# Optimization experiments

Hardware: AMD Instinct MI355X
Metric: run time of the kernel (lower is better)

The kernel has to match this reference:

```python
import jax, jax.numpy as jnp
import numpy as np

B, N, X, H = 128, 512, 128, 256  # batch, seq len, in features, hidden

_PARAM_SHAPES = [
    ("fg_w_c", (H,)), ("fg_w_h", (H, H)), ("fg_w_x", (H, X)), ("fg_b", (H,)),
    ("ig_w_c", (H,)), ("ig_w_h", (H, H)), ("ig_w_x", (H, X)), ("ig_b", (H,)),
    ("in_w_h", (H, H)), ("in_w_x", (H, X)), ("in_b", (H,)),
    ("og_w_cn", (H,)), ("og_w_h", (H, H)), ("og_w_x", (H, X)), ("og_b", (H,)), ("og_w_t", (H,)),
    ("tg1_w_x", (H, X)), ("tg1_w_t", (H,)), ("tg1_b", (H,)),
    ("tg2_w_x", (H, X)), ("tg2_w_t", (H,)), ("tg2_b", (H,)),
]


def setup_inputs() -> dict:
    key = jax.random.key(0)
    ks = jax.random.split(key, 2 + len(_PARAM_SHAPES))
    stdv = 1.0 / np.sqrt(H)  # torch __init__ re-inits all params uniform(-stdv, stdv)
    inp = {
        "x": jax.random.normal(ks[0], (B, N, X), jnp.float32),
        "t": jax.random.uniform(ks[1], (B, N, 1), jnp.float32),  # time intervals >= 0
    }
    for i, (name, shape) in enumerate(_PARAM_SHAPES):
        inp[name] = jax.random.uniform(ks[2 + i], shape, jnp.float32, -stdv, stdv)
    return inp


def reference(x, t,
              fg_w_c, fg_w_h, fg_w_x, fg_b,
              ig_w_c, ig_w_h, ig_w_x, ig_b,
              in_w_h, in_w_x, in_b,
              og_w_cn, og_w_h, og_w_x, og_b, og_w_t,
              tg1_w_x, tg1_w_t, tg1_b,
              tg2_w_x, tg2_w_t, tg2_b):
    # TimeLSTM_v3 with nn_type = NN_TYPE_LSTM_TIME2.
    # torch stores vector params as [H,1] and x_cur as [B,xm,1]; here squeezed to [H] / [B,xm].
    # Precompute all input-dependent (non-recurrent) gate terms over the whole sequence: [B,N,H]
    fg_x = jnp.einsum('bnx,hx->bnh', x, fg_w_x) + fg_b
    ig_x = jnp.einsum('bnx,hx->bnh', x, ig_w_x) + ig_b
    in_x = jnp.einsum('bnx,hx->bnh', x, in_w_x) + in_b
    og_x = jnp.einsum('bnx,hx->bnh', x, og_w_x) + og_w_t * t + og_b
    # Time gates depend only on x and t -> fully precomputable
    tm1 = jax.nn.sigmoid(jnp.einsum('bnx,hx->bnh', x, tg1_w_x) + jnp.tanh(tg1_w_t * t) + tg1_b)
    tm2 = jax.nn.sigmoid(jnp.einsum('bnx,hx->bnh', x, tg2_w_x) + jnp.tanh(tg2_w_t * t) + tg2_b)

    def step(carry, inputs):
        h, cm = carry  # each [B,H]
        fg_xt, ig_xt, in_xt, og_xt, tm1_t, tm2_t = inputs
        ig = jax.nn.sigmoid(ig_w_c * cm + h @ ig_w_h.T + ig_xt)
        fg = jax.nn.sigmoid(fg_w_c * cm + h @ fg_w_h.T + fg_xt)
        inn = jnp.tanh(h @ in_w_h.T + in_xt)
        cm_hat = fg * cm + ig * tm1_t * inn
        cm_new = fg * cm + ig * tm2_t * inn
        og = jax.nn.sigmoid(og_w_cn * cm_hat + h @ og_w_h.T + og_xt)
        h_new = og * jnp.tanh(cm_hat)
        return (h_new, cm_new), None

    seqs = tuple(jnp.moveaxis(a, 1, 0) for a in (fg_x, ig_x, in_x, og_x, tm1, tm2))  # [N,B,H]
    init = (jnp.zeros((x.shape[0], H), x.dtype), jnp.zeros((x.shape[0], H), x.dtype))
    (h, cm), _ = jax.lax.scan(step, init, seqs)
    return h, cm  # h: [B,H] (torch squeezes trailing 1), cm: [B,H]
```

## Files before the change

### kernel.cpp

```cpp
#include <hip/hip_runtime.h>
#include <math.h>

#define BATCH 128
#define SEQN  512
#define XF    128
#define HF    256
#define BC    16
#define HC    8
#define TCH   8
#define NBLK  256
#define NTHR  256
#define NGRP  8
#define GSZ   32

#define OFF_WX   0
#define OFF_G    6144
#define OFF_X    12288
#define OFF_CM   28672
#define OFF_TV   28800
#define OFF_COEF 28928
#define OFF_GO   29024
#define LDS_WORDS 29028
#define LDS_BYTES (LDS_WORDS * 4)

struct Params {
  const float* x;
  const float* t;
  const float* w_h[4];
  const float* w_x[6];
  const float* coef[12];
  float* h_buf;
  unsigned* flags;
  float* out;
};

__device__ __forceinline__ float sigmoidf_(float v) { return 1.0f / (1.0f + __expf(-v)); }

__device__ __forceinline__ float swzx1(float v) { return __int_as_float(__builtin_amdgcn_ds_swizzle(__float_as_int(v), 0x041F)); }
__device__ __forceinline__ float swzx2(float v) { return __int_as_float(__builtin_amdgcn_ds_swizzle(__float_as_int(v), 0x081F)); }
__device__ __forceinline__ float swzx4(float v) { return __int_as_float(__builtin_amdgcn_ds_swizzle(__float_as_int(v), 0x101F)); }
__device__ __forceinline__ float swzx8(float v) { return __int_as_float(__builtin_amdgcn_ds_swizzle(__float_as_int(v), 0x201F)); }

__device__ __forceinline__ void post_arrive(unsigned* flags, int gi, int mi, unsigned val) {
  __syncthreads();
  if (threadIdx.x == 0) {
    __hip_atomic_store(&flags[(gi * GSZ + mi) * 16], val,
                       __ATOMIC_RELAXED, __HIP_MEMORY_SCOPE_AGENT);
  }
}

__device__ __forceinline__ void wave_wait(float* sm, const unsigned* flags,
                                          int gi, unsigned target) {
  unsigned* go = (unsigned*)&sm[OFF_GO];
  const int tid = threadIdx.x;
  if (tid < 64) {
    const bool need = tid < GSZ;
    const unsigned* f = &flags[(gi * GSZ + (tid & (GSZ - 1))) * 16];
    while (true) {
      unsigned v = need ? __hip_atomic_load(f, __ATOMIC_RELAXED, __HIP_MEMORY_SCOPE_AGENT)
                        : target;
      if (__all((int)(v >= target))) break;
    }
    if (tid == 0)
      __hip_atomic_store(go, target, __ATOMIC_RELAXED, __HIP_MEMORY_SCOPE_WORKGROUP);
  } else {
    while (__hip_atomic_load(go, __ATOMIC_RELAXED, __HIP_MEMORY_SCOPE_WORKGROUP) < target) {}
  }
  asm volatile("" ::: "memory");
}

__global__ __launch_bounds__(NTHR, 1) void timelstm_kernel(Params p) {
  extern __shared__ float sm[];
  const int tid = threadIdx.x;
  const int bid = blockIdx.x;
  const int gi = bid & 7;
  const int mi = bid >> 3;
  const int b0 = gi * BC;
  const int h0 = mi * HC;

  const int lane = tid & 63;
  const int bq = tid >> 6;
  const int kh = lane & 7;
  const int j  = lane >> 3;

  float wrs[4][32];
#pragma unroll
  for (int g = 0; g < 4; ++g)
#pragma unroll
    for (int q = 0; q < 8; ++q) {
      const float4 v = *(const float4*)&p.w_h[g][(size_t)(h0 + j) * HF + kh * 32 + q * 4];
      wrs[g][q * 4 + 0] = v.x; wrs[g][q * 4 + 1] = v.y;
      wrs[g][q * 4 + 2] = v.z; wrs[g][q * 4 + 3] = v.w;
    }
  for (int i = tid; i < 6 * 8 * 128; i += NTHR) {
    int g = i >> 10, jj = (i >> 7) & 7, k = i & 127;
    sm[OFF_WX + k * 48 + jj * 6 + g] = p.w_x[g][(h0 + jj) * XF + k];
  }
  if (tid < 96) sm[OFF_COEF + tid] = p.coef[tid >> 3][h0 + (tid & 7)];
  if (tid < 128) sm[OFF_CM + tid] = 0.0f;
  if (tid == 0) *(unsigned*)&sm[OFF_GO] = 0u;
  if (mi == 0) {
    unsigned long long* hbu = (unsigned long long*)p.h_buf + (size_t)b0 * (HF / 2);
    for (int i = tid; i < BC * HF / 2; i += NTHR) {
      __hip_atomic_store(&hbu[i], 0ull, __ATOMIC_RELAXED, __HIP_MEMORY_SCOPE_AGENT);
    }
  }
  post_arrive(p.flags, gi, mi, 1u);
  unsigned tstep = 1;
  int cur = 0;

  for (int tc0 = 0; tc0 < SEQN; tc0 += TCH) {
    __syncthreads();
    {
#pragma unroll
      for (int half = 0; half < 2; ++half) {
        float4 xr[8];
#pragma unroll
        for (int it = 0; it < 8; ++it) {
          const int ri = (half * 8 + it) * 8 + (tid >> 5);
          xr[it] = *(const float4*)&p.x[((size_t)(b0 + (ri >> 3)) * SEQN + (tc0 + (ri & 7))) * XF + (tid & 31) * 4];
        }
#pragma unroll
        for (int it = 0; it < 8; ++it) {
          const int ri = (half * 8 + it) * 8 + (tid >> 5);
          const int k0 = (tid & 31) * 4;
          const float xb[4] = {xr[it].x, xr[it].y, xr[it].z, xr[it].w};
#pragma unroll
          for (int u = 0; u < 4; ++u) {
            const int k = k0 + u;
            sm[OFF_X + k * 128 + (ri ^ (((k >> 2) & 7) << 2))] = xb[u];
          }
        }
      }
      if (tid < 128)
        sm[OFF_TV + tid] = p.t[(size_t)(b0 + (tid >> 3)) * SEQN + tc0 + (tid & 7)];
    }
    __syncthreads();
    {
      const int c = tid >> 3, r = tid & 7;
      const int c4 = c << 2;
      float a0[4], a1[4], a2[4], a3[4], a4[4], a5[4];
#pragma unroll
      for (int u = 0; u < 4; ++u) { a0[u]=0.f; a1[u]=0.f; a2[u]=0.f; a3[u]=0.f; a4[u]=0.f; a5[u]=0.f; }
      const float* wxp = &sm[OFF_WX + r * 6];
#pragma unroll 4
      for (int k = 0; k < XF; ++k) {
        const float4 xv = *(const float4*)&sm[OFF_X + k * 128 + (c4 ^ (((k >> 2) & 7) << 2))];
        const float2 wA = *(const float2*)&wxp[k * 48 + 0];
        const float2 wB = *(const float2*)&wxp[k * 48 + 2];
        const float2 wC = *(const float2*)&wxp[k * 48 + 4];
        const float xs[4] = {xv.x, xv.y, xv.z, xv.w};
#pragma unroll
        for (int u = 0; u < 4; ++u) {
          a0[u] += wA.x * xs[u]; a1[u] += wA.y * xs[u];
          a2[u] += wB.x * xs[u]; a3[u] += wB.y * xs[u];
          a4[u] += wC.x * xs[u]; a5[u] += wC.y * xs[u];
        }
      }
      const float cfg  = sm[OFF_COEF + 0 * 8 + r], cig  = sm[OFF_COEF + 1 * 8 + r];
      const float cin  = sm[OFF_COEF + 2 * 8 + r];
      const float cogb = sm[OFF_COEF + 3 * 8 + r], cogwt = sm[OFF_COEF + 4 * 8 + r];
      const float ct1w = sm[OFF_COEF + 5 * 8 + r], ct1b = sm[OFF_COEF + 6 * 8 + r];
      const float ct2w = sm[OFF_COEF + 7 * 8 + r], ct2b = sm[OFF_COEF + 8 * 8 + r];
#pragma unroll
      for (int u = 0; u < 4; ++u) {
        const int bt = c4 + u, b = bt >> 3, t = bt & 7;
        const float tv = sm[OFF_TV + bt];
        float* gp = &sm[OFF_G + t * 768 + b * 8 + r];
        gp[0]   = a0[u] + cfg;
        gp[128] = a1[u] + cig;
        gp[256] = a2[u] + cin;
        gp[384] = a3[u] + cogwt * tv + cogb;
        gp[512] = sigmoidf_(a4[u] + tanhf(ct1w * tv) + ct1b);
        gp[640] = sigmoidf_(a5[u] + tanhf(ct2w * tv) + ct2b);
      }
    }
    __syncthreads();

    for (int tt = 0; tt < TCH; ++tt) {
      wave_wait(sm, p.flags, gi, tstep);
      {
        const unsigned long long* hsrc = (const unsigned long long*)
            (p.h_buf + (size_t)cur * BATCH * HF + (size_t)(b0 + (bq << 2)) * HF);
        unsigned long long v[4][2];
#pragma unroll
        for (int u = 0; u < 4; ++u) {
          const unsigned long long* src = hsrc + (size_t)u * (HF / 2) + lane * 2;
          v[u][0] = __hip_atomic_load(src,     __ATOMIC_RELAXED, __HIP_MEMORY_SCOPE_AGENT);
          v[u][1] = __hip_atomic_load(src + 1, __ATOMIC_RELAXED, __HIP_MEMORY_SCOPE_AGENT);
        }
        float f[4][4];
#pragma unroll
        for (int u = 0; u < 4; ++u) {
          union { unsigned long long u64; float2 f2; } c0, c1;
          c0.u64 = v[u][0]; c1.u64 = v[u][1];
          f[u][0] = c0.f2.x; f[u][1] = c0.f2.y; f[u][2] = c1.f2.x; f[u][3] = c1.f2.y;
        }
        const int swz = ((lane >> 3) & 7) << 2;
        const int wbase = OFF_X + (bq << 10);
#pragma unroll
        for (int e = 0; e < 4; ++e) {
          const int a = wbase + (((lane << 4) + (e << 2)) ^ swz);
          float2 lo = {f[0][e], f[1][e]};
          float2 hi = {f[2][e], f[3][e]};
          *(float2*)&sm[a]     = lo;
          *(float2*)&sm[a + 2] = hi;
        }
      }

      float acc[4][4];
#pragma unroll
      for (int bi = 0; bi < 4; ++bi)
#pragma unroll
        for (int g = 0; g < 4; ++g) acc[bi][g] = 0.f;

      const int hbase = OFF_X + (bq << 10) + (kh << 7);
      const int khx = kh << 2;
#pragma unroll
      for (int kk = 0; kk < 32; ++kk) {
        const int off = ((((kk & 7) << 2) ^ khx)) + ((kk >> 3) << 5);
        const float4 hv = *(const float4*)&sm[hbase + off];
        const float w0 = wrs[0][kk], w1 = wrs[1][kk], w2 = wrs[2][kk], w3 = wrs[3][kk];
        acc[0][0] += hv.x * w0; acc[0][1] += hv.x * w1; acc[0][2] += hv.x * w2; acc[0][3] += hv.x * w3;
        acc[1][0] += hv.y * w0; acc[1][1] += hv.y * w1; acc[1][2] += hv.y * w2; acc[1][3] += hv.y * w3;
        acc[2][0] += hv.z * w0; acc[2][1] += hv.z * w1; acc[2][2] += hv.z * w2; acc[2][3] += hv.z * w3;
        acc[3][0] += hv.w * w0; acc[3][1] += hv.w * w1; acc[3][2] += hv.w * w2; acc[3][3] += hv.w * w3;
      }

      const int kb0 = kh & 1, kb1 = (kh >> 1) & 1;
      float s1[2][4];
#pragma unroll
      for (int pp = 0; pp < 2; ++pp)
#pragma unroll
        for (int g = 0; g < 4; ++g) {
          const float mine  = kb0 ? acc[2 * pp + 1][g] : acc[2 * pp][g];
          const float yours = kb0 ? acc[2 * pp][g]     : acc[2 * pp + 1][g];
          s1[pp][g] = mine + swzx1(yours);
        }
      float s2[4];
#pragma unroll
      for (int g = 0; g < 4; ++g) {
        const float mine  = kb1 ? s1[1][g] : s1[0][g];
        const float yours = kb1 ? s1[0][g] : s1[1][g];
        s2[g] = mine + swzx2(yours);
      }
      float pre[4];
#pragma unroll
      for (int g = 0; g < 4; ++g) pre[g] = s2[g] + swzx4(s2[g]);

      {
        const int bi = kh & 3;
        const int b  = (bq << 2) + bi;
        const int ib = b * 8 + j;
        const float cm = sm[OFF_CM + ib];
        const float* gt = &sm[OFF_G + tt * 768 + ib];
        const float fgx = gt[0],   igx = gt[128], inx = gt[256];
        const float ogx = gt[384], tm1 = gt[512], tm2 = gt[640];
        const float igv = sigmoidf_(sm[OFF_COEF + 10 * 8 + j] * cm + pre[1] + igx);
        const float fgv = sigmoidf_(sm[OFF_COEF + 9 * 8 + j] * cm + pre[0] + fgx);
        const float inn = tanhf(pre[2] + inx);
        const float cbase = fgv * cm, cinn = igv * inn;
        const float cmh = cbase + cinn * tm1;
        const float cmn = cbase + cinn * tm2;
        const float ogv = sigmoidf_(sm[OFF_COEF + 11 * 8 + j] * cmh + pre[3] + ogx);
        const float hn  = ogv * tanhf(cmh);
        const float hn2 = swzx8(hn);
        if (kh < 4) {
          sm[OFF_CM + ib] = cmn;
          if (!(j & 1)) {
            union { float2 f; unsigned long long u; } cv;
            cv.f.x = hn; cv.f.y = hn2;
            unsigned long long* hdst =
                (unsigned long long*)(p.h_buf + (size_t)(cur ^ 1) * BATCH * HF +
                                      (size_t)(b0 + b) * HF + h0 + j);
            __hip_atomic_store(hdst, cv.u, __ATOMIC_RELAXED, __HIP_MEMORY_SCOPE_AGENT);
          }
          if (tc0 + tt == SEQN - 1) {
            p.out[(size_t)(b0 + b) * HF + h0 + j] = hn;
            p.out[(size_t)BATCH * HF + (size_t)(b0 + b) * HF + h0 + j] = cmn;
          }
        }
      }
      post_arrive(p.flags, gi, mi, tstep + 1);
      ++tstep;
      cur ^= 1;
    }
  }
}

extern "C" void kernel_launch(void* const* d_in, const int* in_sizes, int n_in,
                              void* d_out, int out_size, void* d_ws, size_t ws_size,
                              hipStream_t stream) {
  (void)in_sizes; (void)n_in; (void)out_size; (void)ws_size;
  Params p;
  p.x = (const float*)d_in[0];
  p.t = (const float*)d_in[1];
  p.w_h[0] = (const float*)d_in[3];
  p.w_h[1] = (const float*)d_in[7];
  p.w_h[2] = (const float*)d_in[10];
  p.w_h[3] = (const float*)d_in[14];
  p.w_x[0] = (const float*)d_in[4];
  p.w_x[1] = (const float*)d_in[8];
  p.w_x[2] = (const float*)d_in[11];
  p.w_x[3] = (const float*)d_in[15];
  p.w_x[4] = (const float*)d_in[18];
  p.w_x[5] = (const float*)d_in[21];
  p.coef[0]  = (const float*)d_in[5];
  p.coef[1]  = (const float*)d_in[9];
  p.coef[2]  = (const float*)d_in[12];
  p.coef[3]  = (const float*)d_in[16];
  p.coef[4]  = (const float*)d_in[17];
  p.coef[5]  = (const float*)d_in[19];
  p.coef[6]  = (const float*)d_in[20];
  p.coef[7]  = (const float*)d_in[22];
  p.coef[8]  = (const float*)d_in[23];
  p.coef[9]  = (const float*)d_in[2];
  p.coef[10] = (const float*)d_in[6];
  p.coef[11] = (const float*)d_in[13];
  p.flags = (unsigned*)d_ws;
  p.h_buf = (float*)((char*)d_ws + 32768);
  p.out = (float*)d_out;

  (void)hipMemsetAsync(d_ws, 0, 16384, stream);
  (void)hipFuncSetAttribute((const void*)timelstm_kernel,
                            hipFuncAttributeMaxDynamicSharedMemorySize, LDS_BYTES);
  timelstm_kernel<<<dim3(NBLK), dim3(NTHR), LDS_BYTES, stream>>>(p);
}
```

Baseline: 2.613 ms.

## Overlap next-chunk input projection with inter-block spin waits

Before, the kernel stopped the recurrence at the start of every 8-step chunk to load x and compute the input-gate projections. Now that work is split into 20 slices: x/t loads first, then 8-wide k-chunks of the projection GEMV. Each wave runs pending slices while it spins on the cross-block step flags, so it does useful work during synchronisation idle time instead of at a separate barrier-fenced phase. x staging gets its own LDS region, separate from the h buffer, so both can be live at once. tanhf is also replaced by an exp-based fast tanh. The slices read LDS data written by other waves with no workgroup barrier between them, which risks ordering races, and the fast tanh slightly changes accuracy.

```diff
diff --git a/kernel.cpp b/kernel.cpp
--- a/kernel.cpp
+++ b/kernel.cpp
@@ -12,15 +12,16 @@
 #define NTHR  256
 #define NGRP  8
 #define GSZ   32
+#define NS    20
 
 #define OFF_WX   0
 #define OFF_G    6144
-#define OFF_X    12288
-#define OFF_CM   28672
-#define OFF_TV   28800
-#define OFF_COEF 28928
-#define OFF_GO   29024
-#define LDS_WORDS 29028
+#define OFF_XS   12288
+#define OFF_H    28672
+#define OFF_CM   32768
+#define OFF_COEF 32896
+#define OFF_GO   32992
+#define LDS_WORDS 32996
 #define LDS_BYTES (LDS_WORDS * 4)
 
 struct Params {
@@ -35,6 +36,10 @@
 };
 
 __device__ __forceinline__ float sigmoidf_(float v) { return 1.0f / (1.0f + __expf(-v)); }
+__device__ __forceinline__ float tanhf_(float x) {
+  const float e = __expf(2.0f * x);
+  return 1.0f - 2.0f / (e + 1.0f);
+}
 
 __device__ __forceinline__ float swzx1(float v) { return __int_as_float(__builtin_amdgcn_ds_swizzle(__float_as_int(v), 0x041F)); }
 __device__ __forceinline__ float swzx2(float v) { return __int_as_float(__builtin_amdgcn_ds_swizzle(__float_as_int(v), 0x081F)); }
@@ -47,26 +52,6 @@
     __hip_atomic_store(&flags[(gi * GSZ + mi) * 16], val,
                        __ATOMIC_RELAXED, __HIP_MEMORY_SCOPE_AGENT);
   }
-}
-
-__device__ __forceinline__ void wave_wait(float* sm, const unsigned* flags,
-                                          int gi, unsigned target) {
-  unsigned* go = (unsigned*)&sm[OFF_GO];
-  const int tid = threadIdx.x;
-  if (tid < 64) {
-    const bool need = tid < GSZ;
-    const unsigned* f = &flags[(gi * GSZ + (tid & (GSZ - 1))) * 16];
-    while (true) {
-      unsigned v = need ? __hip_atomic_load(f, __ATOMIC_RELAXED, __HIP_MEMORY_SCOPE_AGENT)
-                        : target;
-      if (__all((int)(v >= target))) break;
-    }
-    if (tid == 0)
-      __hip_atomic_store(go, target, __ATOMIC_RELAXED, __HIP_MEMORY_SCOPE_WORKGROUP);
-  } else {
-    while (__hip_atomic_load(go, __ATOMIC_RELAXED, __HIP_MEMORY_SCOPE_WORKGROUP) < target) {}
-  }
-  asm volatile("" ::: "memory");
 }
 
 __global__ __launch_bounds__(NTHR, 1) void timelstm_kernel(Params p) {
@@ -106,46 +91,51 @@
     }
   }
   post_arrive(p.flags, gi, mi, 1u);
-  unsigned tstep = 1;
-  int cur = 0;
-
-  for (int tc0 = 0; tc0 < SEQN; tc0 += TCH) {
-    __syncthreads();
-    {
-#pragma unroll
-      for (int half = 0; half < 2; ++half) {
-        float4 xr[8];
-#pragma unroll
-        for (int it = 0; it < 8; ++it) {
-          const int ri = (half * 8 + it) * 8 + (tid >> 5);
-          xr[it] = *(const float4*)&p.x[((size_t)(b0 + (ri >> 3)) * SEQN + (tc0 + (ri & 7))) * XF + (tid & 31) * 4];
-        }
-#pragma unroll
-        for (int it = 0; it < 8; ++it) {
-          const int ri = (half * 8 + it) * 8 + (tid >> 5);
-          const int k0 = (tid & 31) * 4;
-          const float xb[4] = {xr[it].x, xr[it].y, xr[it].z, xr[it].w};
-#pragma unroll
-          for (int u = 0; u < 4; ++u) {
-            const int k = k0 + u;
-            sm[OFF_X + k * 128 + (ri ^ (((k >> 2) & 7) << 2))] = xb[u];
-          }
-        }
-      }
-      if (tid < 128)
-        sm[OFF_TV + tid] = p.t[(size_t)(b0 + (tid >> 3)) * SEQN + tc0 + (tid & 7)];
-    }
-    __syncthreads();
-    {
-      const int c = tid >> 3, r = tid & 7;
-      const int c4 = c << 2;
-      float a0[4], a1[4], a2[4], a3[4], a4[4], a5[4];
-#pragma unroll
-      for (int u = 0; u < 4; ++u) { a0[u]=0.f; a1[u]=0.f; a2[u]=0.f; a3[u]=0.f; a4[u]=0.f; a5[u]=0.f; }
-      const float* wxp = &sm[OFF_WX + r * 6];
-#pragma unroll 4
-      for (int k = 0; k < XF; ++k) {
-        const float4 xv = *(const float4*)&sm[OFF_X + k * 128 + (c4 ^ (((k >> 2) & 7) << 2))];
+
+  float a0[4], a1[4], a2[4], a3[4], a4[4], a5[4];
+  float tvr[4];
+#pragma unroll
+  for (int u = 0; u < 4; ++u) { a0[u]=0.f; a1[u]=0.f; a2[u]=0.f; a3[u]=0.f; a4[u]=0.f; a5[u]=0.f; }
+  int tc_next = 0;
+  int sc = 0;
+  const int cc = tid >> 3, rr = tid & 7;
+  const int c4 = cc << 2;
+
+  auto do_slice = [&](int s) {
+    if (s < 4) {
+      if (s == 0) {
+#pragma unroll
+        for (int u = 0; u < 4; ++u) {
+          const int bt = c4 + u;
+          tvr[u] = p.t[(size_t)(b0 + (bt >> 3)) * SEQN + tc_next + (bt & 7)];
+        }
+      }
+      float4 xr[4];
+#pragma unroll
+      for (int q = 0; q < 4; ++q) {
+        const int it = s * 4 + q;
+        const int bt = (bq << 5) + it * 2 + (lane >> 5);
+        xr[q] = *(const float4*)&p.x[((size_t)(b0 + (bt >> 3)) * SEQN + (tc_next + (bt & 7))) * XF + (lane & 31) * 4];
+      }
+#pragma unroll
+      for (int q = 0; q < 4; ++q) {
+        const int it = s * 4 + q;
+        const int bt = (bq << 5) + it * 2 + (lane >> 5);
+        const int k0 = (lane & 31) * 4;
+        const float xb[4] = {xr[q].x, xr[q].y, xr[q].z, xr[q].w};
+#pragma unroll
+        for (int u = 0; u < 4; ++u) {
+          const int k = k0 + u;
+          sm[OFF_XS + k * 128 + (bt ^ (((k >> 2) & 7) << 2))] = xb[u];
+        }
+      }
+    } else {
+      const float* wxp = &sm[OFF_WX + rr * 6];
+      const int kbase = (s - 4) * 8;
+#pragma unroll
+      for (int kk = 0; kk < 8; ++kk) {
+        const int k = kbase + kk;
+        const float4 xv = *(const float4*)&sm[OFF_XS + k * 128 + (c4 ^ (((k >> 2) & 7) << 2))];
         const float2 wA = *(const float2*)&wxp[k * 48 + 0];
         const float2 wB = *(const float2*)&wxp[k * 48 + 2];
         const float2 wC = *(const float2*)&wxp[k * 48 + 4];
@@ -157,28 +147,65 @@
           a4[u] += wC.x * xs[u]; a5[u] += wC.y * xs[u];
         }
       }
-      const float cfg  = sm[OFF_COEF + 0 * 8 + r], cig  = sm[OFF_COEF + 1 * 8 + r];
-      const float cin  = sm[OFF_COEF + 2 * 8 + r];
-      const float cogb = sm[OFF_COEF + 3 * 8 + r], cogwt = sm[OFF_COEF + 4 * 8 + r];
-      const float ct1w = sm[OFF_COEF + 5 * 8 + r], ct1b = sm[OFF_COEF + 6 * 8 + r];
-      const float ct2w = sm[OFF_COEF + 7 * 8 + r], ct2b = sm[OFF_COEF + 8 * 8 + r];
-#pragma unroll
-      for (int u = 0; u < 4; ++u) {
-        const int bt = c4 + u, b = bt >> 3, t = bt & 7;
-        const float tv = sm[OFF_TV + bt];
-        float* gp = &sm[OFF_G + t * 768 + b * 8 + r];
-        gp[0]   = a0[u] + cfg;
-        gp[128] = a1[u] + cig;
-        gp[256] = a2[u] + cin;
-        gp[384] = a3[u] + cogwt * tv + cogb;
-        gp[512] = sigmoidf_(a4[u] + tanhf(ct1w * tv) + ct1b);
-        gp[640] = sigmoidf_(a5[u] + tanhf(ct2w * tv) + ct2b);
-      }
-    }
-    __syncthreads();
+    }
+  };
+
+  auto dump_G = [&]() {
+    const float cfg  = sm[OFF_COEF + 0 * 8 + rr], cig  = sm[OFF_COEF + 1 * 8 + rr];
+    const float cin  = sm[OFF_COEF + 2 * 8 + rr];
+    const float cogb = sm[OFF_COEF + 3 * 8 + rr], cogwt = sm[OFF_COEF + 4 * 8 + rr];
+    const float ct1w = sm[OFF_COEF + 5 * 8 + rr], ct1b = sm[OFF_COEF + 6 * 8 + rr];
+    const float ct2w = sm[OFF_COEF + 7 * 8 + rr], ct2b = sm[OFF_COEF + 8 * 8 + rr];
+#pragma unroll
+    for (int u = 0; u < 4; ++u) {
+      const int bt = c4 + u, b = bt >> 3, t = bt & 7;
+      const float tv = tvr[u];
+      float* gp = &sm[OFF_G + t * 768 + b * 8 + rr];
+      gp[0]   = a0[u] + cfg;
+      gp[128] = a1[u] + cig;
+      gp[256] = a2[u] + cin;
+      gp[384] = a3[u] + cogwt * tv + cogb;
+      gp[512] = sigmoidf_(a4[u] + tanhf_(ct1w * tv) + ct1b);
+      gp[640] = sigmoidf_(a5[u] + tanhf_(ct2w * tv) + ct2b);
+      a0[u] = 0.f; a1[u] = 0.f; a2[u] = 0.f; a3[u] = 0.f; a4[u] = 0.f; a5[u] = 0.f;
+    }
+  };
+
+  auto wave_wait_s = [&](unsigned target) {
+    unsigned* go = (unsigned*)&sm[OFF_GO];
+    if (tid < 64) {
+      const bool need = tid < GSZ;
+      const unsigned* f = &p.flags[(gi * GSZ + (tid & (GSZ - 1))) * 16];
+      while (true) {
+        unsigned v = need ? __hip_atomic_load(f, __ATOMIC_RELAXED, __HIP_MEMORY_SCOPE_AGENT)
+                          : target;
+        if (__all((int)(v >= target))) break;
+        if (sc < NS) { do_slice(sc); ++sc; }
+      }
+      if (tid == 0)
+        __hip_atomic_store(go, target, __ATOMIC_RELAXED, __HIP_MEMORY_SCOPE_WORKGROUP);
+    } else {
+      while (true) {
+        unsigned v = __hip_atomic_load(go, __ATOMIC_RELAXED, __HIP_MEMORY_SCOPE_WORKGROUP);
+        if (v >= target) break;
+        if (sc < NS) { do_slice(sc); ++sc; }
+      }
+    }
+    asm volatile("" ::: "memory");
+  };
+
+  for (int s = 0; s < NS; ++s) do_slice(s);
+  dump_G();
+
+  unsigned tstep = 1;
+  int cur = 0;
+
+  for (int tc0 = 0; tc0 < SEQN; tc0 += TCH) {
+    tc_next = tc0 + TCH;
+    sc = (tc_next < SEQN) ? 0 : NS;
 
     for (int tt = 0; tt < TCH; ++tt) {
-      wave_wait(sm, p.flags, gi, tstep);
+      wave_wait_s(tstep);
       {
         const unsigned long long* hsrc = (const unsigned long long*)
             (p.h_buf + (size_t)cur * BATCH * HF + (size_t)(b0 + (bq << 2)) * HF);
@@ -192,12 +219,12 @@
         float f[4][4];
 #pragma unroll
         for (int u = 0; u < 4; ++u) {
-          union { unsigned long long u64; float2 f2; } c0, c1;
-          c0.u64 = v[u][0]; c1.u64 = v[u][1];
-          f[u][0] = c0.f2.x; f[u][1] = c0.f2.y; f[u][2] = c1.f2.x; f[u][3] = c1.f2.y;
+          union { unsigned long long u64; float2 f2; } x0, x1;
+          x0.u64 = v[u][0]; x1.u64 = v[u][1];
+          f[u][0] = x0.f2.x; f[u][1] = x0.f2.y; f[u][2] = x1.f2.x; f[u][3] = x1.f2.y;
         }
         const int swz = ((lane >> 3) & 7) << 2;
-        const int wbase = OFF_X + (bq << 10);
+        const int wbase = OFF_H + (bq << 10);
 #pragma unroll
         for (int e = 0; e < 4; ++e) {
           const int a = wbase + (((lane << 4) + (e << 2)) ^ swz);
@@ -214,7 +241,7 @@
 #pragma unroll
         for (int g = 0; g < 4; ++g) acc[bi][g] = 0.f;
 
-      const int hbase = OFF_X + (bq << 10) + (kh << 7);
+      const int hbase = OFF_H + (bq << 10) + (kh << 7);
       const int khx = kh << 2;
 #pragma unroll
       for (int kk = 0; kk < 32; ++kk) {
@@ -258,12 +285,12 @@
         const float ogx = gt[384], tm1 = gt[512], tm2 = gt[640];
         const float igv = sigmoidf_(sm[OFF_COEF + 10 * 8 + j] * cm + pre[1] + igx);
         const float fgv = sigmoidf_(sm[OFF_COEF + 9 * 8 + j] * cm + pre[0] + fgx);
-        const float inn = tanhf(pre[2] + inx);
+        const float inn = tanhf_(pre[2] + inx);
         const float cbase = fgv * cm, cinn = igv * inn;
         const float cmh = cbase + cinn * tm1;
         const float cmn = cbase + cinn * tm2;
         const float ogv = sigmoidf_(sm[OFF_COEF + 11 * 8 + j] * cmh + pre[3] + ogx);
-        const float hn  = ogv * tanhf(cmh);
+        const float hn  = ogv * tanhf_(cmh);
         const float hn2 = swzx8(hn);
         if (kh < 4) {
           sm[OFF_CM + ib] = cmn;
@@ -284,6 +311,11 @@
       post_arrive(p.flags, gi, mi, tstep + 1);
       ++tstep;
       cur ^= 1;
+    }
+
+    if (tc_next < SEQN) {
+      while (sc < NS) { do_slice(sc); ++sc; }
+      dump_G();
     }
   }
 }
```

Measured after the change: 2.874 ms. 10.0% more time.

## Use leader-block round counter for group barrier and fast exp-based tanh

Applied to the files above, without the earlier changes.

Per-step group synchronization changes from every block polling all 32 peer flags to only the mi==0 block polling them. That block then publishes a per-group round counter, and the other blocks spin on that single word. This cuts the polling traffic on the flags but adds an extra hop of latency through the leader block on the critical recurrence path. It also replaces tanhf with an __expf-based tanh to shorten the gate math, at some cost in accuracy and overflow behaviour for large inputs.

```diff
diff --git a/kernel.cpp b/kernel.cpp
--- a/kernel.cpp
+++ b/kernel.cpp
@@ -31,10 +31,15 @@
   const float* coef[12];
   float* h_buf;
   unsigned* flags;
+  unsigned* round;
   float* out;
 };
 
 __device__ __forceinline__ float sigmoidf_(float v) { return 1.0f / (1.0f + __expf(-v)); }
+__device__ __forceinline__ float tanhf_(float x) {
+  const float e = __expf(2.0f * x);
+  return 1.0f - 2.0f / (e + 1.0f);
+}
 
 __device__ __forceinline__ float swzx1(float v) { return __int_as_float(__builtin_amdgcn_ds_swizzle(__float_as_int(v), 0x041F)); }
 __device__ __forceinline__ float swzx2(float v) { return __int_as_float(__builtin_amdgcn_ds_swizzle(__float_as_int(v), 0x081F)); }
@@ -50,21 +55,30 @@
 }
 
 __device__ __forceinline__ void wave_wait(float* sm, const unsigned* flags,
-                                          int gi, unsigned target) {
-  unsigned* go = (unsigned*)&sm[OFF_GO];
+                                          unsigned* round, int gi, int mi,
+                                          unsigned target) {
   const int tid = threadIdx.x;
-  if (tid < 64) {
-    const bool need = tid < GSZ;
-    const unsigned* f = &flags[(gi * GSZ + (tid & (GSZ - 1))) * 16];
-    while (true) {
-      unsigned v = need ? __hip_atomic_load(f, __ATOMIC_RELAXED, __HIP_MEMORY_SCOPE_AGENT)
-                        : target;
-      if (__all((int)(v >= target))) break;
-    }
-    if (tid == 0)
-      __hip_atomic_store(go, target, __ATOMIC_RELAXED, __HIP_MEMORY_SCOPE_WORKGROUP);
+  if (mi == 0) {
+    unsigned* go = (unsigned*)&sm[OFF_GO];
+    if (tid < 64) {
+      const bool need = tid < GSZ;
+      const unsigned* f = &flags[(gi * GSZ + (tid & (GSZ - 1))) * 16];
+      while (true) {
+        unsigned v = need ? __hip_atomic_load(f, __ATOMIC_RELAXED, __HIP_MEMORY_SCOPE_AGENT)
+                          : target;
+        if (__all((int)(v >= target))) break;
+      }
+      if (tid == 0) {
+        __hip_atomic_store(&round[gi * 16], target,
+                           __ATOMIC_RELAXED, __HIP_MEMORY_SCOPE_AGENT);
+        __hip_atomic_store(go, target, __ATOMIC_RELAXED, __HIP_MEMORY_SCOPE_WORKGROUP);
+      }
+    } else {
+      while (__hip_atomic_load(go, __ATOMIC_RELAXED, __HIP_MEMORY_SCOPE_WORKGROUP) < target) {}
+    }
   } else {
-    while (__hip_atomic_load(go, __ATOMIC_RELAXED, __HIP_MEMORY_SCOPE_WORKGROUP) < target) {}
+    const unsigned* r = &round[gi * 16];
+    while (__hip_atomic_load(r, __ATOMIC_RELAXED, __HIP_MEMORY_SCOPE_AGENT) < target) {}
   }
   asm volatile("" ::: "memory");
 }
@@ -171,14 +185,14 @@
         gp[128] = a1[u] + cig;
         gp[256] = a2[u] + cin;
         gp[384] = a3[u] + cogwt * tv + cogb;
-        gp[512] = sigmoidf_(a4[u] + tanhf(ct1w * tv) + ct1b);
-        gp[640] = sigmoidf_(a5[u] + tanhf(ct2w * tv) + ct2b);
+        gp[512] = sigmoidf_(a4[u] + tanhf_(ct1w * tv) + ct1b);
+        gp[640] = sigmoidf_(a5[u] + tanhf_(ct2w * tv) + ct2b);
       }
     }
     __syncthreads();
 
     for (int tt = 0; tt < TCH; ++tt) {
-      wave_wait(sm, p.flags, gi, tstep);
+      wave_wait(sm, p.flags, p.round, gi, mi, tstep);
       {
         const unsigned long long* hsrc = (const unsigned long long*)
             (p.h_buf + (size_t)cur * BATCH * HF + (size_t)(b0 + (bq << 2)) * HF);
@@ -192,9 +206,9 @@
         float f[4][4];
 #pragma unroll
         for (int u = 0; u < 4; ++u) {
-          union { unsigned long long u64; float2 f2; } c0, c1;
-          c0.u64 = v[u][0]; c1.u64 = v[u][1];
-          f[u][0] = c0.f2.x; f[u][1] = c0.f2.y; f[u][2] = c1.f2.x; f[u][3] = c1.f2.y;
+          union { unsigned long long u64; float2 f2; } x0, x1;
+          x0.u64 = v[u][0]; x1.u64 = v[u][1];
+          f[u][0] = x0.f2.x; f[u][1] = x0.f2.y; f[u][2] = x1.f2.x; f[u][3] = x1.f2.y;
         }
         const int swz = ((lane >> 3) & 7) << 2;
         const int wbase = OFF_X + (bq << 10);
@@ -258,12 +272,12 @@
         const float ogx = gt[384], tm1 = gt[512], tm2 = gt[640];
         const float igv = sigmoidf_(sm[OFF_COEF + 10 * 8 + j] * cm + pre[1] + igx);
         const float fgv = sigmoidf_(sm[OFF_COEF + 9 * 8 + j] * cm + pre[0] + fgx);
-        const float inn = tanhf(pre[2] + inx);
+        const float inn = tanhf_(pre[2] + inx);
         const float cbase = fgv * cm, cinn = igv * inn;
         const float cmh = cbase + cinn * tm1;
         const float cmn = cbase + cinn * tm2;
         const float ogv = sigmoidf_(sm[OFF_COEF + 11 * 8 + j] * cmh + pre[3] + ogx);
-        const float hn  = ogv * tanhf(cmh);
+        const float hn  = ogv * tanhf_(cmh);
         const float hn2 = swzx8(hn);
         if (kh < 4) {
           sm[OFF_CM + ib] = cmn;
@@ -318,10 +332,11 @@
   p.coef[10] = (const float*)d_in[6];
   p.coef[11] = (const float*)d_in[13];
   p.flags = (unsigned*)d_ws;
+  p.round = p.flags + NGRP * GSZ * 16;
   p.h_buf = (float*)((char*)d_ws + 32768);
   p.out = (float*)d_out;
 
-  (void)hipMemsetAsync(d_ws, 0, 16384, stream);
+  (void)hipMemsetAsync(d_ws, 0, 32768, stream);
   (void)hipFuncSetAttribute((const void*)timelstm_kernel,
                             hipFuncAttributeMaxDynamicSharedMemorySize, LDS_BYTES);
   timelstm_kernel<<<dim3(NBLK), dim3(NTHR), LDS_BYTES, stream>>>(p);
```

After: 2.633 ms (median of 2 runs). About the same (+0.8%).
